# Kernel tuning notes

Measured on AMD Instinct MI355X. Metric: run time of the kernel, lower is better.

## Reference

```python
import jax, jax.numpy as jnp
import numpy as np

B, C, H, W = 16, 3, 224, 224
P = 16
DIM = 256
NL = 8
DS = 16          # d_state (mamba default)
DCONV = 4
NCLS = 1000
DI = 2 * DIM     # expand * dim
DTR = -(-DIM // 16)  # dt_rank = ceil(dim/16)
NPATCH = (H // P) * (W // P)
SEQ = NPATCH + 1


def _ln(x, g, b, eps=1e-5):
    mu = x.mean(-1, keepdims=True)
    var = ((x - mu) ** 2).mean(-1, keepdims=True)
    return (x - mu) * jax.lax.rsqrt(var + eps) * g + b


def setup_inputs() -> dict:
    key = jax.random.key(0)
    ks = jax.random.split(key, 12)
    pd = C * P * P
    s = 0.02
    return dict(
        img=jax.random.normal(ks[0], (B, C, H, W), jnp.float32),
        pe_ln1_g=jnp.ones((pd,), jnp.float32), pe_ln1_b=jnp.zeros((pd,), jnp.float32),
        pe_w=jax.random.normal(ks[1], (pd, DIM), jnp.float32) * s,
        pe_b=jnp.zeros((DIM,), jnp.float32),
        pe_ln2_g=jnp.ones((DIM,), jnp.float32), pe_ln2_b=jnp.zeros((DIM,), jnp.float32),
        pos_emb=jax.random.normal(ks[2], (1, SEQ, DIM), jnp.float32) * s,
        cls_tok=jax.random.normal(ks[3], (1, 1, DIM), jnp.float32) * s,
        ln_w=jnp.ones((NL, DIM), jnp.float32), ln_b=jnp.zeros((NL, DIM), jnp.float32),
        in_w=jax.random.normal(ks[4], (NL, DIM, 2 * DI), jnp.float32) * s,
        conv_w=jax.random.normal(ks[5], (NL, DI, DCONV), jnp.float32) * s,
        conv_b=jnp.zeros((NL, DI), jnp.float32),
        xproj_w=jax.random.normal(ks[6], (NL, DI, DTR + 2 * DS), jnp.float32) * s,
        dtproj_w=jax.random.normal(ks[7], (NL, DTR, DI), jnp.float32) * s,
        dtproj_b=jax.random.uniform(ks[8], (NL, DI), jnp.float32, -4.0, -2.0),
        A_log=jnp.log(jnp.broadcast_to(jnp.arange(1, DS + 1, dtype=jnp.float32), (NL, DI, DS))) + jnp.zeros((NL, DI, DS), jnp.float32),
        Dp=jnp.ones((NL, DI), jnp.float32),
        out_w=jax.random.normal(ks[9], (NL, DI, DIM), jnp.float32) * s,
        normf_w=jnp.ones((DIM,), jnp.float32), normf_b=jnp.zeros((DIM,), jnp.float32),
        head_w=jax.random.normal(ks[10], (DIM, NCLS), jnp.float32) * s,
        head_b=jnp.zeros((NCLS,), jnp.float32),
    )


def _mamba(x, in_w, conv_w, conv_b, xproj_w, dtproj_w, dtproj_b, A_log, Dp, out_w):
    b, L, _ = x.shape
    xz = x @ in_w                       # (b, L, 2*DI)
    xm, z = jnp.split(xz, 2, axis=-1)
    # causal depthwise conv1d (torch pads both sides then slices -> left-pad d_conv-1)
    xc = jnp.pad(xm.transpose(0, 2, 1), ((0, 0), (0, 0), (DCONV - 1, 0)))
    xc = jax.lax.conv_general_dilated(
        xc, conv_w[:, None, :], (1,), 'VALID',
        dimension_numbers=('NCH', 'OIH', 'NCH'), feature_group_count=DI)
    u = jax.nn.silu(xc + conv_b[None, :, None]).transpose(0, 2, 1)  # (b, L, DI)
    dbc = u @ xproj_w                   # (b, L, DTR+2*DS)
    dt, Bm, Cm = jnp.split(dbc, [DTR, DTR + DS], axis=-1)
    dt = jax.nn.softplus(dt @ dtproj_w + dtproj_b)  # (b, L, DI)
    A = -jnp.exp(A_log)                 # (DI, DS)

    def step(h, inp):
        dt_t, B_t, C_t, u_t = inp       # (b,DI), (b,DS), (b,DS), (b,DI)
        dA = jnp.exp(dt_t[:, :, None] * A)                 # (b, DI, DS)
        h = dA * h + (dt_t * u_t)[:, :, None] * B_t[:, None, :]
        y = jnp.einsum('bdn,bn->bd', h, C_t)
        return h, y

    h0 = jnp.zeros((b, DI, DS), x.dtype)
    xs = (dt.transpose(1, 0, 2), Bm.transpose(1, 0, 2),
          Cm.transpose(1, 0, 2), u.transpose(1, 0, 2))
    _, ys = jax.lax.scan(step, h0, xs)
    y = ys.transpose(1, 0, 2) + u * Dp  # (b, L, DI)
    y = y * jax.nn.silu(z)
    return y @ out_w                    # (b, L, DIM)


def reference(img, pe_ln1_g, pe_ln1_b, pe_w, pe_b, pe_ln2_g, pe_ln2_b, pos_emb,
              cls_tok, ln_w, ln_b, in_w, conv_w, conv_b, xproj_w, dtproj_w,
              dtproj_b, A_log, Dp, out_w, normf_w, normf_b, head_w, head_b):
    b = img.shape[0]
    h, w = H // P, W // P
    # 'b c (h p1) (w p2) -> b (h w) (p1 p2 c)'
    x = img.reshape(b, C, h, P, w, P).transpose(0, 2, 4, 3, 5, 1).reshape(b, h * w, P * P * C)
    x = _ln(x, pe_ln1_g, pe_ln1_b)
    x = x @ pe_w + pe_b
    x = _ln(x, pe_ln2_g, pe_ln2_b)
    x = jnp.concatenate([jnp.broadcast_to(cls_tok, (b, 1, DIM)), x], axis=1)
    x = x + pos_emb[:, :x.shape[1]]
    residual = None
    for i in range(NL):
        residual = x if residual is None else x + residual
        xn = _ln(residual, ln_w[i], ln_b[i])
        x = _mamba(xn, in_w[i], conv_w[i], conv_b[i], xproj_w[i],
                   dtproj_w[i], dtproj_b[i], A_log[i], Dp[i], out_w[i])
    residual = x + residual
    x = _ln(residual, normf_w, normf_b)
    x = x[:, 0]                          # pool == 'cls'
    return x @ head_w + head_b
```

## Files before the change

### kernel.cpp

```cpp
#include <hip/hip_runtime.h>
#include <math.h>

#define NB   16
#define SEQL 197
#define TB   (NB*SEQL)
#define DIMM 256
#define DI   512
#define DS   16
#define NL   8

typedef __bf16 bf16x8 __attribute__((ext_vector_type(8)));
typedef __bf16 bf16x4 __attribute__((ext_vector_type(4)));
typedef float floatx4 __attribute__((ext_vector_type(4)));

__device__ __forceinline__ void block_reduce_2(float& s1, float& s2, float* red, int tid){
  #pragma unroll
  for (int off = 32; off > 0; off >>= 1){
    s1 += __shfl_down(s1, off, 64);
    s2 += __shfl_down(s2, off, 64);
  }
  __syncthreads();
  if ((tid & 63) == 0){ red[(tid>>6)*2] = s1; red[(tid>>6)*2+1] = s2; }
  __syncthreads();
  s1 = red[0] + red[2] + red[4] + red[6];
  s2 = red[1] + red[3] + red[5] + red[7];
}

__global__ __launch_bounds__(256) void transpose_bf16(
    const float* __restrict__ in, __bf16* __restrict__ out, int K, int N)
{
  __shared__ float t[32][33];
  const float* src = in  + (size_t)blockIdx.z*K*N;
  __bf16*      dst = out + (size_t)blockIdx.z*K*N;
  int n0 = blockIdx.x*32, k0 = blockIdx.y*32;
  int tx = threadIdx.x & 31, ty = threadIdx.x >> 5;
  #pragma unroll
  for (int j = 0; j < 4; j++)
    t[ty + j*8][tx] = src[(size_t)(k0 + ty + j*8)*N + n0 + tx];
  __syncthreads();
  #pragma unroll
  for (int j = 0; j < 4; j++)
    dst[(size_t)(n0 + ty + j*8)*K + k0 + tx] = (__bf16)t[tx][ty + j*8];
}

__global__ __launch_bounds__(256) void transpose_bf16_pad(
    const float* __restrict__ in, __bf16* __restrict__ out, int K, int Nin, int Npad)
{
  __shared__ float t[32][33];
  const float* src = in  + (size_t)blockIdx.z*K*Nin;
  __bf16*      dst = out + (size_t)blockIdx.z*Npad*K;
  int n0 = blockIdx.x*32, k0 = blockIdx.y*32;
  int tx = threadIdx.x & 31, ty = threadIdx.x >> 5;
  #pragma unroll
  for (int j = 0; j < 4; j++){
    int n = n0 + tx;
    t[ty + j*8][tx] = (n < Nin) ? src[(size_t)(k0 + ty + j*8)*Nin + n] : 0.f;
  }
  __syncthreads();
  #pragma unroll
  for (int j = 0; j < 4; j++)
    dst[(size_t)(n0 + ty + j*8)*K + k0 + tx] = (__bf16)t[tx][ty + j*8];
}

template<int BM, int BN, int KS>
__global__ __launch_bounds__(256) void gemm_bf16(
    const __bf16* __restrict__ A, const __bf16* __restrict__ Wt,
    const float* __restrict__ bias, float* __restrict__ C, int M, int N, int K)
{
  constexpr int BK  = 32;
  constexpr int LDA = BK + 8;
  constexpr int TMW = BM/32;
  constexpr int TNW = BN/32;
  __shared__ __bf16 As[BM][LDA];
  __shared__ __bf16 Bs[BN][LDA];

  int tid  = threadIdx.x;
  int lane = tid & 63, w = tid >> 6;
  int wm = w >> 1, wn = w & 1;
  int l15 = lane & 15, quad = lane >> 4;
  int nt = blockIdx.x / KS, ks = blockIdx.x % KS;
  int bm = blockIdx.y * BM, bn = nt * BN;
  int kbeg = ks * (K / KS), kend = kbeg + (K / KS);

  floatx4 acc[TMW][TNW] = {};

  for (int k0 = kbeg; k0 < kend; k0 += BK){
    #pragma unroll
    for (int i = 0; i < BM/64; i++){
      int c = tid + i*256;
      int row = c >> 2, kc = c & 3;
      int m = bm + row;
      uint4 v = make_uint4(0,0,0,0);
      if (m < M) v = ((const uint4*)(A + (size_t)m*K + k0))[kc];
      *(uint4*)&As[row][kc*8] = v;
    }
    #pragma unroll
    for (int i = 0; i < BN/64; i++){
      int c = tid + i*256;
      int row = c >> 2, kc = c & 3;
      int n = bn + row;
      uint4 v = ((const uint4*)(Wt + (size_t)n*K + k0))[kc];
      *(uint4*)&Bs[row][kc*8] = v;
    }
    __syncthreads();
    bf16x8 af[TMW], bf[TNW];
    #pragma unroll
    for (int mi = 0; mi < TMW; mi++)
      af[mi] = *(const bf16x8*)&As[wm*(BM/2) + mi*16 + l15][quad*8];
    #pragma unroll
    for (int ni = 0; ni < TNW; ni++)
      bf[ni] = *(const bf16x8*)&Bs[wn*(BN/2) + ni*16 + l15][quad*8];
    #pragma unroll
    for (int mi = 0; mi < TMW; mi++)
      #pragma unroll
      for (int ni = 0; ni < TNW; ni++)
        acc[mi][ni] = __builtin_amdgcn_mfma_f32_16x16x32_bf16(af[mi], bf[ni], acc[mi][ni], 0, 0, 0);
    __syncthreads();
  }
  #pragma unroll
  for (int mi = 0; mi < TMW; mi++){
    #pragma unroll
    for (int ni = 0; ni < TNW; ni++){
      int col = bn + wn*(BN/2) + ni*16 + l15;
      float bv = (KS == 1 && bias) ? bias[col] : 0.f;
      #pragma unroll
      for (int r = 0; r < 4; r++){
        int row = bm + wm*(BM/2) + mi*16 + quad*4 + r;
        if (row < M){
          if (KS == 1) C[(size_t)row*N + col] = acc[mi][ni][r] + bv;
          else         atomicAdd(&C[(size_t)row*N + col], acc[mi][ni][r]);
        }
      }
    }
  }
}

__global__ __launch_bounds__(256) void patch_ln1(
    const float* __restrict__ img, const float* __restrict__ g1, const float* __restrict__ b1,
    __bf16* __restrict__ xp_bf)
{
  __shared__ float red[8];
  int blk = blockIdx.x;
  int b = blk / 196, p = blk % 196;
  int hh = p / 14, ww = p % 14;
  int tid = threadIdx.x;

  float v[3]; float s = 0.f, s2 = 0.f;
  #pragma unroll
  for (int i = 0; i < 3; i++){
    int e  = tid + i*256;
    int c  = e % 3;
    int p2 = (e/3) % 16;
    int p1 = e / 48;
    float val = img[((b*3 + c)*224 + hh*16 + p1)*224 + ww*16 + p2];
    v[i] = val; s += val; s2 += val*val;
  }
  block_reduce_2(s, s2, red, tid);
  float mu = s * (1.f/768.f);
  float var = s2 * (1.f/768.f) - mu*mu;
  float rr = rsqrtf(var + 1e-5f);
  #pragma unroll
  for (int i = 0; i < 3; i++){
    int e = tid + i*256;
    xp_bf[(size_t)blk*768 + e] = (__bf16)((v[i] - mu) * rr * g1[e] + b1[e]);
  }
}

__global__ __launch_bounds__(256) void ln2_cls_pos(
    const float* __restrict__ pemb, const float* __restrict__ g2, const float* __restrict__ b2,
    const float* __restrict__ pos, const float* __restrict__ cls, float* __restrict__ x)
{
  __shared__ float red[8];
  int blk = blockIdx.x;
  int b = blk / SEQL, l = blk % SEQL;
  int tid = threadIdx.x;
  if (l == 0){
    x[(size_t)b*SEQL*256 + tid] = cls[tid] + pos[tid];
    return;
  }
  int p = l - 1;
  float v = pemb[(size_t)(b*196 + p)*256 + tid];
  float s = v, s2 = v*v;
  block_reduce_2(s, s2, red, tid);
  float mu = s * (1.f/256.f);
  float var = s2 * (1.f/256.f) - mu*mu;
  float rr = rsqrtf(var + 1e-5f);
  float o = (v - mu) * rr * g2[tid] + b2[tid] + pos[(1+p)*256 + tid];
  x[((size_t)(b*SEQL + 1 + p))*256 + tid] = o;
}

__global__ __launch_bounds__(256) void add_ln(
    const float* __restrict__ x, float* __restrict__ resid, __bf16* __restrict__ xn_bf,
    const float* __restrict__ g, const float* __restrict__ bta, int first)
{
  int w = threadIdx.x >> 6, l = threadIdx.x & 63;
  int t = blockIdx.x*4 + w;
  size_t base = (size_t)t*256 + l*4;
  float4 xv = *(const float4*)&x[base];
  if (!first){
    float4 rv = *(const float4*)&resid[base];
    xv.x += rv.x; xv.y += rv.y; xv.z += rv.z; xv.w += rv.w;
  }
  *(float4*)&resid[base] = xv;
  float s  = xv.x + xv.y + xv.z + xv.w;
  float s2 = xv.x*xv.x + xv.y*xv.y + xv.z*xv.z + xv.w*xv.w;
  #pragma unroll
  for (int off = 1; off < 64; off <<= 1){
    s  += __shfl_xor(s,  off, 64);
    s2 += __shfl_xor(s2, off, 64);
  }
  float mu = s * (1.f/256.f);
  float var = s2 * (1.f/256.f) - mu*mu;
  float rr = rsqrtf(var + 1e-5f);
  float4 gv = *(const float4*)&g[l*4];
  float4 bv = *(const float4*)&bta[l*4];
  bf16x4 o;
  o[0] = (__bf16)((xv.x - mu)*rr*gv.x + bv.x);
  o[1] = (__bf16)((xv.y - mu)*rr*gv.y + bv.y);
  o[2] = (__bf16)((xv.z - mu)*rr*gv.z + bv.z);
  o[3] = (__bf16)((xv.w - mu)*rr*gv.w + bv.w);
  *(bf16x4*)&xn_bf[base] = o;
}

__global__ __launch_bounds__(256) void conv_silu(
    const float* __restrict__ xz, const float* __restrict__ cw, const float* __restrict__ cb,
    float* __restrict__ u, __bf16* __restrict__ u_bf, float* __restrict__ dbc)
{
  int gid = blockIdx.x*256 + threadIdx.x;
  int dq = gid & 127;
  int t = gid >> 7;
  int d = dq*4;
  int l = t % SEQL;
  const float4 z4 = make_float4(0.f,0.f,0.f,0.f);
  if (dq < 16) *(float4*)&dbc[(size_t)t*64 + d] = z4;
  float4 x0 = *(const float4*)&xz[(size_t)t*1024 + d];
  float4 x1 = (l>=1) ? *(const float4*)&xz[(size_t)(t-1)*1024 + d] : z4;
  float4 x2 = (l>=2) ? *(const float4*)&xz[(size_t)(t-2)*1024 + d] : z4;
  float4 x3 = (l>=3) ? *(const float4*)&xz[(size_t)(t-3)*1024 + d] : z4;
  float4 w0 = *(const float4*)&cw[(d+0)*4];
  float4 w1 = *(const float4*)&cw[(d+1)*4];
  float4 w2 = *(const float4*)&cw[(d+2)*4];
  float4 w3 = *(const float4*)&cw[(d+3)*4];
  float4 r = *(const float4*)&cb[d];
  r.x += x3.x*w0.x + x2.x*w0.y + x1.x*w0.z + x0.x*w0.w;
  r.y += x3.y*w1.x + x2.y*w1.y + x1.y*w1.z + x0.y*w1.w;
  r.z += x3.z*w2.x + x2.z*w2.y + x1.z*w2.z + x0.z*w2.w;
  r.w += x3.w*w3.x + x2.w*w3.y + x1.w*w3.z + x0.w*w3.w;
  r.x *= 1.f/(1.f + __expf(-r.x));
  r.y *= 1.f/(1.f + __expf(-r.y));
  r.z *= 1.f/(1.f + __expf(-r.z));
  r.w *= 1.f/(1.f + __expf(-r.w));
  *(float4*)&u[(size_t)t*512 + d] = r;
  bf16x4 o; o[0]=(__bf16)r.x; o[1]=(__bf16)r.y; o[2]=(__bf16)r.z; o[3]=(__bf16)r.w;
  *(bf16x4*)&u_bf[(size_t)t*512 + d] = o;
}

#define SCT 32
#define NCH ((SEQL + SCT - 1)/SCT)
#define NDL 8
__global__ __launch_bounds__(128) void scan_kernel(
    const float* __restrict__ u, const float* __restrict__ dbc,
    const float* __restrict__ xz, const float* __restrict__ A_log, const float* __restrict__ Dp,
    const float* __restrict__ dtw, const float* __restrict__ dtb,
    __bf16* __restrict__ yg_bf)
{
  __shared__ float s_D [16][36];
  __shared__ float s_B [16][36];
  __shared__ float s_C [16][36];
  __shared__ float s_u [NDL][36];
  __shared__ float s_z [NDL][36];
  __shared__ float s_dt[NDL][36];
  __shared__ float s_yp[SCT][NDL][20];
  __shared__ float s_dp[NDL];

  int tid = threadIdx.x;
  int n = tid & 15, dl = tid >> 4;
  int b = blockIdx.x >> 6, dg = blockIdx.x & 63;
  int d0 = dg * NDL;
  const size_t base = (size_t)b * SEQL;

  float A = -__expf(A_log[(d0+dl)*DS + n]);
  float h = 0.f;
  if (tid < NDL) s_dp[tid] = Dp[d0 + tid];
  int cch = tid & 7;
  float wc[16];
  #pragma unroll
  for (int k = 0; k < 16; k++) wc[k] = dtw[k*512 + d0 + cch];
  float dtbv = dtb[d0 + cch];

  float r_u[2], r_z[2], r_db[12];
  auto load_regs = [&](int c){
    #pragma unroll
    for (int i = 0; i < 2; i++){
      int v = tid + i*128;
      int tg = c*SCT + (v>>3); if (tg > SEQL-1) tg = SEQL-1;
      size_t t = base + tg;
      r_u[i] = u [t*512 + d0 + (v&7)];
      r_z[i] = xz[t*1024 + 512 + d0 + (v&7)];
    }
    #pragma unroll
    for (int s = 0; s < 3; s++)
      #pragma unroll
      for (int i = 0; i < 4; i++){
        int v = tid + i*128;
        int tg = c*SCT + (v>>4); if (tg > SEQL-1) tg = SEQL-1;
        r_db[s*4+i] = dbc[(base + tg)*64 + s*16 + (v&15)];
      }
  };
  auto write_DBC = [&](){
    #pragma unroll
    for (int i = 0; i < 4; i++){
      int v = tid + i*128;
      s_D[v&15][v>>4] = r_db[0+i];
      s_B[v&15][v>>4] = r_db[4+i];
      s_C[v&15][v>>4] = r_db[8+i];
    }
  };
  auto write_UZ = [&](){
    #pragma unroll
    for (int i = 0; i < 2; i++){
      int v = tid + i*128;
      s_u[v&7][v>>3] = r_u[i];
      s_z[v&7][v>>3] = r_z[i];
    }
  };
  auto compute_dt = [&](){
    #pragma unroll
    for (int i = 0; i < 2; i++){
      int tl = (tid >> 3) + i*16;
      float acc = dtbv;
      #pragma unroll
      for (int k = 0; k < 16; k++) acc += s_D[k][tl] * wc[k];
      s_dt[cch][tl] = (acc > 20.f) ? acc : log1pf(__expf(acc));
    }
  };

  load_regs(0);
  write_DBC();
  write_UZ();
  __syncthreads();
  compute_dt();
  __syncthreads();

  for (int c = 0; c < NCH; c++){
    if (c + 1 < NCH) load_regs(c+1);

    float4 dt4, u4, B4, C4;
    #pragma unroll
    for (int tl = 0; tl < SCT; tl++){
      if ((tl & 3) == 0){
        dt4 = *(const float4*)&s_dt[dl][tl];
        u4  = *(const float4*)&s_u [dl][tl];
        B4  = *(const float4*)&s_B [n][tl];
        C4  = *(const float4*)&s_C [n][tl];
      }
      float dtv = ((float*)&dt4)[tl&3];
      float uv  = ((float*)&u4 )[tl&3];
      float Bv  = ((float*)&B4 )[tl&3];
      float Cv  = ((float*)&C4 )[tl&3];
      h = __expf(dtv * A) * h + (dtv * uv) * Bv;
      s_yp[tl][dl][n] = h * Cv;
    }
    __syncthreads();

    if (c + 1 < NCH) write_DBC();

    #pragma unroll
    for (int j = 0; j < 2; j++){
      int p = tid + j*128;
      int tl = p >> 3, dr = p & 7;
      float4 a0 = *(const float4*)&s_yp[tl][dr][0];
      float4 a1 = *(const float4*)&s_yp[tl][dr][4];
      float4 a2 = *(const float4*)&s_yp[tl][dr][8];
      float4 a3 = *(const float4*)&s_yp[tl][dr][12];
      float yv = ((a0.x+a0.y)+(a0.z+a0.w)) + ((a1.x+a1.y)+(a1.z+a1.w))
               + ((a2.x+a2.y)+(a2.z+a2.w)) + ((a3.x+a3.y)+(a3.z+a3.w));
      int tg = c*SCT + tl;
      if (tg < SEQL){
        float uv = s_u[dr][tl];
        float zv = s_z[dr][tl];
        float sg = 1.f / (1.f + __expf(-zv));
        yg_bf[(base + tg)*512 + d0 + dr] = (__bf16)((yv + uv*s_dp[dr]) * zv * sg);
      }
    }
    __syncthreads();

    if (c + 1 < NCH){
      write_UZ();
      compute_dt();
      __syncthreads();
    }
  }
}

__global__ __launch_bounds__(256) void final_ln(
    const float* __restrict__ x, const float* __restrict__ resid,
    const float* __restrict__ g, const float* __restrict__ bta, float* __restrict__ xs_g)
{
  __shared__ float red[8];
  int b = blockIdx.x, tid = threadIdx.x;
  size_t idx = (size_t)b*SEQL*256 + tid;
  float r = x[idx] + resid[idx];
  float s = r, s2 = r*r;
  block_reduce_2(s, s2, red, tid);
  float mu = s * (1.f/256.f);
  float var = s2 * (1.f/256.f) - mu*mu;
  float rr = rsqrtf(var + 1e-5f);
  xs_g[b*256 + tid] = (r - mu) * rr * g[tid] + bta[tid];
}

__global__ __launch_bounds__(256) void head_gemm(
    const float* __restrict__ xs_g, const float* __restrict__ head_w,
    const float* __restrict__ head_b, float* __restrict__ out)
{
  __shared__ float xs[16][256];
  int tid = threadIdx.x;
  #pragma unroll
  for (int i = 0; i < 16; i++) ((float*)xs)[tid + i*256] = xs_g[tid + i*256];
  __syncthreads();
  int nl = tid & 31, bq = tid >> 5;
  int nn = blockIdx.x*32 + nl;
  if (nn >= 1000) return;
  float acc0 = 0.f, acc1 = 0.f;
  #pragma unroll 8
  for (int k = 0; k < 256; k++){
    float w = head_w[k*1000 + nn];
    acc0 += xs[bq][k]   * w;
    acc1 += xs[bq+8][k] * w;
  }
  float hb = head_b[nn];
  out[(size_t)bq*1000 + nn]     = acc0 + hb;
  out[(size_t)(bq+8)*1000 + nn] = acc1 + hb;
}

extern "C" void kernel_launch(void* const* d_in, const int* in_sizes, int n_in,
                              void* d_out, int out_size, void* d_ws, size_t ws_size,
                              hipStream_t stream) {
  const float* img   = (const float*)d_in[0];
  const float* ln1g  = (const float*)d_in[1];
  const float* ln1b  = (const float*)d_in[2];
  const float* pe_w  = (const float*)d_in[3];
  const float* pe_b  = (const float*)d_in[4];
  const float* ln2g  = (const float*)d_in[5];
  const float* ln2b  = (const float*)d_in[6];
  const float* pos   = (const float*)d_in[7];
  const float* cls   = (const float*)d_in[8];
  const float* ln_w  = (const float*)d_in[9];
  const float* ln_b  = (const float*)d_in[10];
  const float* in_w  = (const float*)d_in[11];
  const float* conv_w= (const float*)d_in[12];
  const float* conv_b= (const float*)d_in[13];
  const float* xproj = (const float*)d_in[14];
  const float* dtw   = (const float*)d_in[15];
  const float* dtb   = (const float*)d_in[16];
  const float* A_log = (const float*)d_in[17];
  const float* Dp    = (const float*)d_in[18];
  const float* out_w = (const float*)d_in[19];
  const float* nfw   = (const float*)d_in[20];
  const float* nfb   = (const float*)d_in[21];
  const float* head_w= (const float*)d_in[22];
  const float* head_b= (const float*)d_in[23];
  float* out = (float*)d_out;

  float* ws = (float*)d_ws;
  float* x     = ws;  ws += (size_t)TB*DIMM;
  float* resid = ws;  ws += (size_t)TB*DIMM;
  float* xz    = ws;  ws += (size_t)TB*2*DI;
  float* u     = ws;  ws += (size_t)TB*DI;
  float* dbc   = ws;  ws += (size_t)TB*64;
  float* xs_g  = ws;  ws += (size_t)NB*DIMM;
  __bf16* xn_bf = (__bf16*)ws;  ws += (size_t)TB*DIMM/2;
  __bf16* u_bf  = (__bf16*)ws;  ws += (size_t)TB*DI/2;
  __bf16* yg_bf = (__bf16*)ws;  ws += (size_t)TB*DI/2;
  __bf16* wt_in = (__bf16*)ws;  ws += (size_t)NL*1024*256/2;
  __bf16* wt_out= (__bf16*)ws;  ws += (size_t)NL*256*512/2;
  __bf16* wt_pe = (__bf16*)ws;  ws += (size_t)256*768/2;
  __bf16* wt_xp = (__bf16*)ws;  ws += (size_t)NL*64*512/2;
  __bf16* xp_bf = (__bf16*)xz;
  float*  pemb  = u;

  transpose_bf16<<<dim3(1024/32, 256/32, NL), 256, 0, stream>>>(in_w,  wt_in, 256, 1024);
  transpose_bf16<<<dim3( 256/32, 512/32, NL), 256, 0, stream>>>(out_w, wt_out, 512, 256);
  transpose_bf16<<<dim3( 256/32, 768/32,  1), 256, 0, stream>>>(pe_w,  wt_pe, 768, 256);
  transpose_bf16_pad<<<dim3(2, 512/32, NL), 256, 0, stream>>>(xproj, wt_xp, 512, 48, 64);

  patch_ln1<<<NB*196, 256, 0, stream>>>(img, ln1g, ln1b, xp_bf);
  gemm_bf16<64,64,1><<<dim3(256/64, 3136/64), 256, 0, stream>>>(
      xp_bf, wt_pe, pe_b, pemb, 3136, 256, 768);
  ln2_cls_pos<<<NB*SEQL, 256, 0, stream>>>(pemb, ln2g, ln2b, pos, cls, x);

  for (int i = 0; i < NL; i++){
    add_ln<<<TB/4, 256, 0, stream>>>(x, resid, xn_bf, ln_w + i*DIMM, ln_b + i*DIMM, i == 0 ? 1 : 0);
    gemm_bf16<64,128,1><<<dim3(1024/128, (TB+63)/64), 256, 0, stream>>>(
        xn_bf, wt_in + (size_t)i*1024*256, nullptr, xz, TB, 1024, 256);
    conv_silu<<<TB*128/256, 256, 0, stream>>>(
        xz, conv_w + i*DI*4, conv_b + i*DI, u, u_bf, dbc);
    gemm_bf16<64,64,4><<<dim3(4, (TB+63)/64), 256, 0, stream>>>(
        u_bf, wt_xp + (size_t)i*64*512, nullptr, dbc, TB, 64, 512);
    scan_kernel<<<NB*64, 128, 0, stream>>>(
        u, dbc, xz, A_log + i*DI*DS, Dp + i*DI, dtw + i*16*DI, dtb + i*DI, yg_bf);
    gemm_bf16<64,64,1><<<dim3(4, (TB+63)/64), 256, 0, stream>>>(
        yg_bf, wt_out + (size_t)i*256*512, nullptr, x, TB, DIMM, 512);
  }
  final_ln<<<NB, 256, 0, stream>>>(x, resid, nfw, nfb, xs_g);
  head_gemm<<<(1000+31)/32, 256, 0, stream>>>(xs_g, head_w, head_b, out);
}
```

Before: 683.5 us.

## Fuse residual add and LayerNorm into out-projection GEMM epilogue

Adds a full-row out-projection GEMM (16 rows by all 256 columns per block) whose epilogue adds the residual in place and computes the next layer's LayerNorm. This removes the separate add_ln kernel and the intermediate x buffer. The first layer's norm is folded into ln2_cls_pos, and the four weight-transpose launches are merged into one kernel. The new GEMM runs only 197 blocks of 512 threads with a small M tile, which may underuse the GPU compared with the old tiled GEMM.

Result: faster. 659.1 us (-3.6%).

```diff
diff --git a/kernel.cpp b/kernel.cpp
--- a/kernel.cpp
+++ b/kernel.cpp
@@ -26,30 +26,36 @@
   s2 = red[1] + red[3] + red[5] + red[7];
 }
 
-__global__ __launch_bounds__(256) void transpose_bf16(
-    const float* __restrict__ in, __bf16* __restrict__ out, int K, int N)
+__global__ __launch_bounds__(256) void prep_weights(
+    const float* __restrict__ in_w, const float* __restrict__ out_w,
+    const float* __restrict__ pe_w, const float* __restrict__ xproj,
+    __bf16* __restrict__ wt_in, __bf16* __restrict__ wt_out,
+    __bf16* __restrict__ wt_pe, __bf16* __restrict__ wt_xp)
 {
   __shared__ float t[32][33];
-  const float* src = in  + (size_t)blockIdx.z*K*N;
-  __bf16*      dst = out + (size_t)blockIdx.z*K*N;
-  int n0 = blockIdx.x*32, k0 = blockIdx.y*32;
-  int tx = threadIdx.x & 31, ty = threadIdx.x >> 5;
-  #pragma unroll
-  for (int j = 0; j < 4; j++)
-    t[ty + j*8][tx] = src[(size_t)(k0 + ty + j*8)*N + n0 + tx];
-  __syncthreads();
-  #pragma unroll
-  for (int j = 0; j < 4; j++)
-    dst[(size_t)(n0 + ty + j*8)*K + k0 + tx] = (__bf16)t[tx][ty + j*8];
-}
-
-__global__ __launch_bounds__(256) void transpose_bf16_pad(
-    const float* __restrict__ in, __bf16* __restrict__ out, int K, int Nin, int Npad)
-{
-  __shared__ float t[32][33];
-  const float* src = in  + (size_t)blockIdx.z*K*Nin;
-  __bf16*      dst = out + (size_t)blockIdx.z*Npad*K;
-  int n0 = blockIdx.x*32, k0 = blockIdx.y*32;
+  int bid = blockIdx.x;
+  const float* src; __bf16* dst;
+  int K, Nin, n0, k0;
+  if (bid < 2048){
+    int z = bid >> 8, tt = bid & 255;
+    K = 256; Nin = 1024; n0 = (tt & 31)*32; k0 = (tt >> 5)*32;
+    src = in_w  + (size_t)z*K*Nin;
+    dst = wt_in + (size_t)z*K*Nin;
+  } else if (bid < 3072){
+    int t2 = bid - 2048; int z = t2 >> 7, tt = t2 & 127;
+    K = 512; Nin = 256; n0 = (tt & 7)*32; k0 = (tt >> 3)*32;
+    src = out_w  + (size_t)z*K*Nin;
+    dst = wt_out + (size_t)z*K*Nin;
+  } else if (bid < 3264){
+    int tt = bid - 3072;
+    K = 768; Nin = 256; n0 = (tt & 7)*32; k0 = (tt >> 3)*32;
+    src = pe_w; dst = wt_pe;
+  } else {
+    int t2 = bid - 3264; int z = t2 >> 5, tt = t2 & 31;
+    K = 512; Nin = 48; n0 = (tt & 1)*32; k0 = (tt >> 1)*32;
+    src = xproj + (size_t)z*K*Nin;
+    dst = wt_xp + (size_t)z*64*K;
+  }
   int tx = threadIdx.x & 31, ty = threadIdx.x >> 5;
   #pragma unroll
   for (int j = 0; j < 4; j++){
@@ -135,6 +141,86 @@
   }
 }
 
+template<int DO_LN>
+__global__ __launch_bounds__(512) void gemm_out_fused(
+    const __bf16* __restrict__ A, const __bf16* __restrict__ Wt,
+    float* __restrict__ resid, __bf16* __restrict__ xn_bf,
+    const float* __restrict__ g, const float* __restrict__ bta)
+{
+  constexpr int BK = 64, LDA = BK + 8;
+  __shared__ alignas(16) char smem[(16 + 256) * LDA * sizeof(__bf16)];
+  __bf16 (*As)[LDA] = (__bf16(*)[LDA])smem;
+  __bf16 (*Bs)[LDA] = (__bf16(*)[LDA])(smem + 16*LDA*sizeof(__bf16));
+  float  (*sy)[264] = (float(*)[264])smem;
+
+  int tid = threadIdx.x, lane = tid & 63, w = tid >> 6;
+  int l15 = lane & 15, quad = lane >> 4;
+  int bm = blockIdx.x * 16;
+
+  floatx4 acc[2] = {};
+  for (int k0 = 0; k0 < 512; k0 += BK){
+    if (tid < 128){
+      int row = tid >> 3, kc = tid & 7;
+      *(uint4*)&As[row][kc*8] = ((const uint4*)(A + (size_t)(bm+row)*512 + k0))[kc];
+    }
+    #pragma unroll
+    for (int i = 0; i < 4; i++){
+      int c = tid + i*512;
+      int row = c >> 3, kc = c & 7;
+      *(uint4*)&Bs[row][kc*8] = ((const uint4*)(Wt + (size_t)row*512 + k0))[kc];
+    }
+    __syncthreads();
+    #pragma unroll
+    for (int kk = 0; kk < 2; kk++){
+      bf16x8 af = *(const bf16x8*)&As[l15][kk*32 + quad*8];
+      #pragma unroll
+      for (int ni = 0; ni < 2; ni++){
+        bf16x8 bfv = *(const bf16x8*)&Bs[w*32 + ni*16 + l15][kk*32 + quad*8];
+        acc[ni] = __builtin_amdgcn_mfma_f32_16x16x32_bf16(af, bfv, acc[ni], 0, 0, 0);
+      }
+    }
+    __syncthreads();
+  }
+  #pragma unroll
+  for (int ni = 0; ni < 2; ni++){
+    int col = w*32 + ni*16 + l15;
+    #pragma unroll
+    for (int r = 0; r < 4; r++)
+      sy[quad*4 + r][col] = acc[ni][r];
+  }
+  __syncthreads();
+  #pragma unroll
+  for (int rr = 0; rr < 2; rr++){
+    int row = w*2 + rr;
+    size_t base = (size_t)(bm + row)*256 + lane*4;
+    float4 y4 = *(const float4*)&sy[row][lane*4];
+    float4 rv = *(const float4*)&resid[base];
+    float4 v;
+    v.x = y4.x + rv.x; v.y = y4.y + rv.y; v.z = y4.z + rv.z; v.w = y4.w + rv.w;
+    *(float4*)&resid[base] = v;
+    if (DO_LN){
+      float s  = v.x + v.y + v.z + v.w;
+      float s2 = v.x*v.x + v.y*v.y + v.z*v.z + v.w*v.w;
+      #pragma unroll
+      for (int off = 1; off < 64; off <<= 1){
+        s  += __shfl_xor(s,  off, 64);
+        s2 += __shfl_xor(s2, off, 64);
+      }
+      float mu  = s * (1.f/256.f);
+      float var = s2 * (1.f/256.f) - mu*mu;
+      float rrq = rsqrtf(var + 1e-5f);
+      float4 gv = *(const float4*)&g[lane*4];
+      float4 bv = *(const float4*)&bta[lane*4];
+      bf16x4 o;
+      o[0] = (__bf16)((v.x - mu)*rrq*gv.x + bv.x);
+      o[1] = (__bf16)((v.y - mu)*rrq*gv.y + bv.y);
+      o[2] = (__bf16)((v.z - mu)*rrq*gv.z + bv.z);
+      o[3] = (__bf16)((v.w - mu)*rrq*gv.w + bv.w);
+      *(bf16x4*)&xn_bf[base] = o;
+    }
+  }
+}
+
 __global__ __launch_bounds__(256) void patch_ln1(
     const float* __restrict__ img, const float* __restrict__ g1, const float* __restrict__ b1,
     __bf16* __restrict__ xp_bf)
@@ -168,58 +254,36 @@
 
 __global__ __launch_bounds__(256) void ln2_cls_pos(
     const float* __restrict__ pemb, const float* __restrict__ g2, const float* __restrict__ b2,
-    const float* __restrict__ pos, const float* __restrict__ cls, float* __restrict__ x)
+    const float* __restrict__ pos, const float* __restrict__ cls,
+    float* __restrict__ resid,
+    const float* __restrict__ g0, const float* __restrict__ b0,
+    __bf16* __restrict__ xn_bf)
 {
   __shared__ float red[8];
   int blk = blockIdx.x;
   int b = blk / SEQL, l = blk % SEQL;
   int tid = threadIdx.x;
+  float o;
   if (l == 0){
-    x[(size_t)b*SEQL*256 + tid] = cls[tid] + pos[tid];
-    return;
-  }
-  int p = l - 1;
-  float v = pemb[(size_t)(b*196 + p)*256 + tid];
-  float s = v, s2 = v*v;
+    o = cls[tid] + pos[tid];
+  } else {
+    int p = l - 1;
+    float v = pemb[(size_t)(b*196 + p)*256 + tid];
+    float s = v, s2 = v*v;
+    block_reduce_2(s, s2, red, tid);
+    float mu = s * (1.f/256.f);
+    float var = s2 * (1.f/256.f) - mu*mu;
+    float rr = rsqrtf(var + 1e-5f);
+    o = (v - mu) * rr * g2[tid] + b2[tid] + pos[l*256 + tid];
+  }
+  size_t idx = (size_t)blk*256 + tid;
+  resid[idx] = o;
+  float s = o, s2 = o*o;
   block_reduce_2(s, s2, red, tid);
   float mu = s * (1.f/256.f);
   float var = s2 * (1.f/256.f) - mu*mu;
   float rr = rsqrtf(var + 1e-5f);
-  float o = (v - mu) * rr * g2[tid] + b2[tid] + pos[(1+p)*256 + tid];
-  x[((size_t)(b*SEQL + 1 + p))*256 + tid] = o;
-}
-
-__global__ __launch_bounds__(256) void add_ln(
-    const float* __restrict__ x, float* __restrict__ resid, __bf16* __restrict__ xn_bf,
-    const float* __restrict__ g, const float* __restrict__ bta, int first)
-{
-  int w = threadIdx.x >> 6, l = threadIdx.x & 63;
-  int t = blockIdx.x*4 + w;
-  size_t base = (size_t)t*256 + l*4;
-  float4 xv = *(const float4*)&x[base];
-  if (!first){
-    float4 rv = *(const float4*)&resid[base];
-    xv.x += rv.x; xv.y += rv.y; xv.z += rv.z; xv.w += rv.w;
-  }
-  *(float4*)&resid[base] = xv;
-  float s  = xv.x + xv.y + xv.z + xv.w;
-  float s2 = xv.x*xv.x + xv.y*xv.y + xv.z*xv.z + xv.w*xv.w;
-  #pragma unroll
-  for (int off = 1; off < 64; off <<= 1){
-    s  += __shfl_xor(s,  off, 64);
-    s2 += __shfl_xor(s2, off, 64);
-  }
-  float mu = s * (1.f/256.f);
-  float var = s2 * (1.f/256.f) - mu*mu;
-  float rr = rsqrtf(var + 1e-5f);
-  float4 gv = *(const float4*)&g[l*4];
-  float4 bv = *(const float4*)&bta[l*4];
-  bf16x4 o;
-  o[0] = (__bf16)((xv.x - mu)*rr*gv.x + bv.x);
-  o[1] = (__bf16)((xv.y - mu)*rr*gv.y + bv.y);
-  o[2] = (__bf16)((xv.z - mu)*rr*gv.z + bv.z);
-  o[3] = (__bf16)((xv.w - mu)*rr*gv.w + bv.w);
-  *(bf16x4*)&xn_bf[base] = o;
+  xn_bf[idx] = (__bf16)((o - mu) * rr * g0[tid] + b0[tid]);
 }
 
 __global__ __launch_bounds__(256) void conv_silu(
@@ -394,13 +458,13 @@
 }
 
 __global__ __launch_bounds__(256) void final_ln(
-    const float* __restrict__ x, const float* __restrict__ resid,
+    const float* __restrict__ resid,
     const float* __restrict__ g, const float* __restrict__ bta, float* __restrict__ xs_g)
 {
   __shared__ float red[8];
   int b = blockIdx.x, tid = threadIdx.x;
   size_t idx = (size_t)b*SEQL*256 + tid;
-  float r = x[idx] + resid[idx];
+  float r = resid[idx];
   float s = r, s2 = r*r;
   block_reduce_2(s, s2, red, tid);
   float mu = s * (1.f/256.f);
@@ -463,7 +527,6 @@
   float* out = (float*)d_out;
 
   float* ws = (float*)d_ws;
-  float* x     = ws;  ws += (size_t)TB*DIMM;
   float* resid = ws;  ws += (size_t)TB*DIMM;
   float* xz    = ws;  ws += (size_t)TB*2*DI;
   float* u     = ws;  ws += (size_t)TB*DI;
@@ -479,18 +542,16 @@
   __bf16* xp_bf = (__bf16*)xz;
   float*  pemb  = u;
 
-  transpose_bf16<<<dim3(1024/32, 256/32, NL), 256, 0, stream>>>(in_w,  wt_in, 256, 1024);
-  transpose_bf16<<<dim3( 256/32, 512/32, NL), 256, 0, stream>>>(out_w, wt_out, 512, 256);
-  transpose_bf16<<<dim3( 256/32, 768/32,  1), 256, 0, stream>>>(pe_w,  wt_pe, 768, 256);
-  transpose_bf16_pad<<<dim3(2, 512/32, NL), 256, 0, stream>>>(xproj, wt_xp, 512, 48, 64);
+  prep_weights<<<3520, 256, 0, stream>>>(in_w, out_w, pe_w, xproj,
+                                          wt_in, wt_out, wt_pe, wt_xp);
 
   patch_ln1<<<NB*196, 256, 0, stream>>>(img, ln1g, ln1b, xp_bf);
   gemm_bf16<64,64,1><<<dim3(256/64, 3136/64), 256, 0, stream>>>(
       xp_bf, wt_pe, pe_b, pemb, 3136, 256, 768);
-  ln2_cls_pos<<<NB*SEQL, 256, 0, stream>>>(pemb, ln2g, ln2b, pos, cls, x);
+  ln2_cls_pos<<<NB*SEQL, 256, 0, stream>>>(pemb, ln2g, ln2b, pos, cls,
+                                           resid, ln_w, ln_b, xn_bf);
 
   for (int i = 0; i < NL; i++){
-    add_ln<<<TB/4, 256, 0, stream>>>(x, resid, xn_bf, ln_w + i*DIMM, ln_b + i*DIMM, i == 0 ? 1 : 0);
     gemm_bf16<64,128,1><<<dim3(1024/128, (TB+63)/64), 256, 0, stream>>>(
         xn_bf, wt_in + (size_t)i*1024*256, nullptr, xz, TB, 1024, 256);
     conv_silu<<<TB*128/256, 256, 0, stream>>>(
@@ -499,9 +560,14 @@
         u_bf, wt_xp + (size_t)i*64*512, nullptr, dbc, TB, 64, 512);
     scan_kernel<<<NB*64, 128, 0, stream>>>(
         u, dbc, xz, A_log + i*DI*DS, Dp + i*DI, dtw + i*16*DI, dtb + i*DI, yg_bf);
-    gemm_bf16<64,64,1><<<dim3(4, (TB+63)/64), 256, 0, stream>>>(
-        yg_bf, wt_out + (size_t)i*256*512, nullptr, x, TB, DIMM, 512);
-  }
-  final_ln<<<NB, 256, 0, stream>>>(x, resid, nfw, nfb, xs_g);
+    if (i < NL-1)
+      gemm_out_fused<1><<<TB/16, 512, 0, stream>>>(
+          yg_bf, wt_out + (size_t)i*256*512, resid, xn_bf,
+          ln_w + (i+1)*DIMM, ln_b + (i+1)*DIMM);
+    else
+      gemm_out_fused<0><<<TB/16, 512, 0, stream>>>(
+          yg_bf, wt_out + (size_t)i*256*512, resid, nullptr, nullptr, nullptr);
+  }
+  final_ln<<<NB, 256, 0, stream>>>(resid, nfw, nfb, xs_g);
   head_gemm<<<(1000+31)/32, 256, 0, stream>>>(xs_g, head_w, head_b, out);
 }
```
